# Kernel optimization log

Measured on AMD Instinct MI355X. Metric: run time of the kernel, lower is better.

The kernel has to match this reference:

```python
import jax, jax.numpy as jnp
import numpy as np

B, N, D = 4, 2048, 768
OUT = 768

def setup_inputs() -> dict:
    key = jax.random.key(0)
    k1, k2 = jax.random.split(key)
    x = jax.random.normal(k1, (B, N, D), dtype=jnp.float32)
    kernel = jax.random.normal(k2, (3, D, OUT), dtype=jnp.float32) * 0.02
    return {"x": x, "kernel": kernel}

def reference(x, kernel):
    # Single-head attention with shared QKV kernel stack [3, D, OUT]
    q = jnp.einsum('bnd,do->bno', x, kernel[0])
    k = jnp.einsum('bnd,do->bno', x, kernel[1])
    v = jnp.einsum('bnd,do->bno', x, kernel[2])
    # NOTE: original divides by 64**0.5 == 8 regardless of dims (faithful)
    scores = jnp.einsum('bqo,bko->bqk', q, k) / 8.0
    attn = jax.nn.softmax(scores, axis=-1)
    return jnp.einsum('bqk,bko->bqo', attn, v)
```

## Files before the change

### kernel.cpp

```cpp
#include <hip/hip_runtime.h>
#include <hip/hip_bf16.h>

constexpr int B_ = 4, N_ = 2048, D_ = 768, OUT_ = 768;
constexpr int M_ = B_ * N_;

typedef __attribute__((ext_vector_type(8))) short short8;
typedef __attribute__((ext_vector_type(4))) float floatx4;

__device__ __forceinline__ unsigned short f2bfu(float f) {
    union { __hip_bfloat16 b; unsigned short u; } cv;
    cv.b = __float2bfloat16(f);
    return cv.u;
}

#define GLOAD_LDS16(g, l)                                                     \
    __builtin_amdgcn_global_load_lds(                                         \
        (const __attribute__((address_space(1))) void*)(g),                   \
        (__attribute__((address_space(3))) void*)(l), 16, 0, 0)

#define MFMA_BF16 __builtin_amdgcn_mfma_f32_16x16x32_bf16
#define WAIT_LGKM0 asm volatile("s_waitcnt lgkmcnt(0)" ::: "memory")


template <int NT>
__device__ __forceinline__ void gemm4p(
    const __hip_bfloat16* __restrict__ aG, int lda,
    const __hip_bfloat16* __restrict__ bG, int ldb,
    unsigned short* LDS, floatx4 (&acc)[8][4]) {
    constexpr int ASLOT = 8192, BSLOT = 8192, BUFS = 32768;
    const int tid = threadIdx.x;
    const int wave = tid >> 6, lane = tid & 63;
    const int lrow = lane & 15, kq = lane >> 4;
    const int wm = (wave >> 2) * 128, wn = (wave & 3) * 64;

    const __hip_bfloat16 *sa0, *sa1, *sb0, *sb1;
    {
        const int r0 = tid >> 2, g0 = (tid & 3) ^ (r0 & 3);
        sa0 = aG + (size_t)r0 * lda + g0 * 8;
        sb0 = bG + (size_t)r0 * ldb + g0 * 8;
        const int u1 = 512 + tid, r1 = u1 >> 2, g1 = (u1 & 3) ^ (r1 & 3);
        sa1 = aG + (size_t)r1 * lda + g1 * 8;
        sb1 = bG + (size_t)r1 * ldb + g1 * 8;
    }
    int oa[8], ob[4];
#pragma unroll
    for (int i = 0; i < 8; ++i) {
        const int r = wm + i * 16 + lrow;
        oa[i] = r * 32 + ((kq ^ (r & 3)) * 8);
    }
#pragma unroll
    for (int i = 0; i < 4; ++i) {
        const int r = wn + i * 16 + lrow;
        ob[i] = r * 32 + ((kq ^ (r & 3)) * 8);
    }

#define SA4(tt, kh)                                                          \
    do {                                                                     \
        unsigned short* d_ =                                                 \
            LDS + ((tt) & 1) * BUFS + (kh) * ASLOT + wave * 512;             \
        GLOAD_LDS16(sa0 + (tt) * 64 + (kh) * 32, d_);                        \
        GLOAD_LDS16(sa1 + (tt) * 64 + (kh) * 32, d_ + 4096);                 \
    } while (0)
#define SB4(tt, kh)                                                          \
    do {                                                                     \
        unsigned short* d_ = LDS + ((tt) & 1) * BUFS + 2 * ASLOT +           \
                             (kh) * BSLOT + wave * 512;                      \
        GLOAD_LDS16(sb0 + (tt) * 64 + (kh) * 32, d_);                        \
        GLOAD_LDS16(sb1 + (tt) * 64 + (kh) * 32, d_ + 4096);                 \
    } while (0)

    SA4(0, 0); SB4(0, 0); SA4(0, 1); SB4(0, 1);
    SA4(1, 0); SB4(1, 0); SA4(1, 1);
    asm volatile("s_waitcnt vmcnt(6)" ::: "memory");
    __builtin_amdgcn_s_barrier();
    __builtin_amdgcn_sched_barrier(0);

    for (int t = 0; t < NT; ++t) {
        const unsigned short* Ab = LDS + (t & 1) * BUFS;
        const unsigned short* Bb = Ab + 2 * ASLOT;
        short8 af[8], bf0, bf1;
#pragma unroll
        for (int i = 0; i < 8; ++i) af[i] = *(const short8*)(Ab + oa[i]);
        bf0 = *(const short8*)(Bb + ob[0]);
        bf1 = *(const short8*)(Bb + ob[1]);
        if (t + 1 < NT) SB4(t + 1, 1);
        __builtin_amdgcn_s_barrier();
        WAIT_LGKM0;
        __builtin_amdgcn_sched_barrier(0);
        __builtin_amdgcn_s_setprio(1);
#pragma unroll
        for (int mi = 0; mi < 8; ++mi) {
            acc[mi][0] = MFMA_BF16(af[mi], bf0, acc[mi][0], 0, 0, 0);
            acc[mi][1] = MFMA_BF16(af[mi], bf1, acc[mi][1], 0, 0, 0);
        }
        __builtin_amdgcn_s_setprio(0);
        __builtin_amdgcn_s_barrier();
        bf0 = *(const short8*)(Bb + ob[2]);
        bf1 = *(const short8*)(Bb + ob[3]);
        if (t + 2 < NT) SA4(t + 2, 0);
        __builtin_amdgcn_s_barrier();
        WAIT_LGKM0;
        __builtin_amdgcn_sched_barrier(0);
        __builtin_amdgcn_s_setprio(1);
#pragma unroll
        for (int mi = 0; mi < 8; ++mi) {
            acc[mi][2] = MFMA_BF16(af[mi], bf0, acc[mi][2], 0, 0, 0);
            acc[mi][3] = MFMA_BF16(af[mi], bf1, acc[mi][3], 0, 0, 0);
        }
        __builtin_amdgcn_s_setprio(0);
        __builtin_amdgcn_s_barrier();
#pragma unroll
        for (int i = 0; i < 8; ++i)
            af[i] = *(const short8*)(Ab + ASLOT + oa[i]);
        bf0 = *(const short8*)(Bb + BSLOT + ob[2]);
        bf1 = *(const short8*)(Bb + BSLOT + ob[3]);
        if (t + 2 < NT) SB4(t + 2, 0);
        __builtin_amdgcn_s_barrier();
        WAIT_LGKM0;
        __builtin_amdgcn_sched_barrier(0);
        __builtin_amdgcn_s_setprio(1);
#pragma unroll
        for (int mi = 0; mi < 8; ++mi) {
            acc[mi][2] = MFMA_BF16(af[mi], bf0, acc[mi][2], 0, 0, 0);
            acc[mi][3] = MFMA_BF16(af[mi], bf1, acc[mi][3], 0, 0, 0);
        }
        __builtin_amdgcn_s_setprio(0);
        __builtin_amdgcn_s_barrier();
        bf0 = *(const short8*)(Bb + BSLOT + ob[0]);
        bf1 = *(const short8*)(Bb + BSLOT + ob[1]);
        if (t + 2 < NT) SA4(t + 2, 1);
        __builtin_amdgcn_s_barrier();
        WAIT_LGKM0;
        __builtin_amdgcn_sched_barrier(0);
        __builtin_amdgcn_s_setprio(1);
#pragma unroll
        for (int mi = 0; mi < 8; ++mi) {
            acc[mi][0] = MFMA_BF16(af[mi], bf0, acc[mi][0], 0, 0, 0);
            acc[mi][1] = MFMA_BF16(af[mi], bf1, acc[mi][1], 0, 0, 0);
        }
        __builtin_amdgcn_s_setprio(0);
        if (t + 2 < NT)
            asm volatile("s_waitcnt vmcnt(6)" ::: "memory");
        else if (t + 1 < NT)
            asm volatile("s_waitcnt vmcnt(0)" ::: "memory");
        __builtin_amdgcn_s_barrier();
        __builtin_amdgcn_sched_barrier(0);
    }
#undef SA4
#undef SB4
}

template <int NT>
__device__ __forceinline__ void gemm2p(
    const __hip_bfloat16* __restrict__ aG, int lda,
    const __hip_bfloat16* __restrict__ bG, int ldb,
    unsigned short* LDS, floatx4 (&acc)[4][4]) {
    constexpr int ASLOT = 4096, BSLOT = 8192, BUFS = 24576;
    const int tid = threadIdx.x;
    const int wave = tid >> 6, lane = tid & 63;
    const int lrow = lane & 15, kq = lane >> 4;
    const int wm = (wave >> 2) * 64, wn = (wave & 3) * 64;

    const __hip_bfloat16 *sa0, *sb0, *sb1;
    {
        const int r0 = tid >> 2, g0 = (tid & 3) ^ (r0 & 3);
        sa0 = aG + (size_t)r0 * lda + g0 * 8;
        sb0 = bG + (size_t)r0 * ldb + g0 * 8;
        const int u1 = 512 + tid, r1 = u1 >> 2, g1 = (u1 & 3) ^ (r1 & 3);
        sb1 = bG + (size_t)r1 * ldb + g1 * 8;
    }
    int oa[4], ob[4];
#pragma unroll
    for (int i = 0; i < 4; ++i) {
        const int ra = wm + i * 16 + lrow;
        oa[i] = ra * 32 + ((kq ^ (ra & 3)) * 8);
        const int rb = wn + i * 16 + lrow;
        ob[i] = rb * 32 + ((kq ^ (rb & 3)) * 8);
    }

#define SA2(tt, kh)                                                          \
    GLOAD_LDS16(sa0 + (tt) * 64 + (kh) * 32,                                 \
                LDS + ((tt) & 1) * BUFS + (kh) * ASLOT + wave * 512)
#define SB2(tt, kh)                                                          \
    do {                                                                     \
        unsigned short* d_ = LDS + ((tt) & 1) * BUFS + 2 * ASLOT +           \
                             (kh) * BSLOT + wave * 512;                      \
        GLOAD_LDS16(sb0 + (tt) * 64 + (kh) * 32, d_);                        \
        GLOAD_LDS16(sb1 + (tt) * 64 + (kh) * 32, d_ + 4096);                 \
    } while (0)

    SA2(0, 0); SB2(0, 0);
    SA2(0, 1); SB2(0, 1);
    SA2(1, 0); SB2(1, 0);
    asm volatile("s_waitcnt vmcnt(3)" ::: "memory");
    __builtin_amdgcn_s_barrier();
    __builtin_amdgcn_sched_barrier(0);

    for (int t = 0; t < NT; ++t) {
        const unsigned short* Ab = LDS + (t & 1) * BUFS;
        const unsigned short* Bb = Ab + 2 * ASLOT;
        short8 af[4], bf[4];
#pragma unroll
        for (int i = 0; i < 4; ++i) af[i] = *(const short8*)(Ab + oa[i]);
#pragma unroll
        for (int i = 0; i < 4; ++i) bf[i] = *(const short8*)(Bb + ob[i]);
        if (t + 1 < NT) { SA2(t + 1, 1); SB2(t + 1, 1); }
        __builtin_amdgcn_s_barrier();
        WAIT_LGKM0;
        __builtin_amdgcn_sched_barrier(0);
        __builtin_amdgcn_s_setprio(1);
#pragma unroll
        for (int mi = 0; mi < 4; ++mi)
#pragma unroll
            for (int ni = 0; ni < 4; ++ni)
                acc[mi][ni] = MFMA_BF16(af[mi], bf[ni], acc[mi][ni], 0, 0, 0);
        __builtin_amdgcn_s_setprio(0);
        __builtin_amdgcn_s_barrier();
#pragma unroll
        for (int i = 0; i < 4; ++i)
            af[i] = *(const short8*)(Ab + ASLOT + oa[i]);
#pragma unroll
        for (int i = 0; i < 4; ++i)
            bf[i] = *(const short8*)(Bb + BSLOT + ob[i]);
        if (t + 2 < NT) { SA2(t + 2, 0); SB2(t + 2, 0); }
        __builtin_amdgcn_s_barrier();
        WAIT_LGKM0;
        __builtin_amdgcn_sched_barrier(0);
        __builtin_amdgcn_s_setprio(1);
#pragma unroll
        for (int mi = 0; mi < 4; ++mi)
#pragma unroll
            for (int ni = 0; ni < 4; ++ni)
                acc[mi][ni] = MFMA_BF16(af[mi], bf[ni], acc[mi][ni], 0, 0, 0);
        __builtin_amdgcn_s_setprio(0);
        if (t + 2 < NT)
            asm volatile("s_waitcnt vmcnt(3)" ::: "memory");
        else if (t + 1 < NT)
            asm volatile("s_waitcnt vmcnt(0)" ::: "memory");
        __builtin_amdgcn_s_barrier();
        __builtin_amdgcn_sched_barrier(0);
    }
#undef SA2
#undef SB2
}

__global__ __launch_bounds__(256)
void prep(const float* __restrict__ x, const float* __restrict__ w,
          __hip_bfloat16* __restrict__ xb, __hip_bfloat16* __restrict__ wt,
          float* __restrict__ l) {
    __shared__ float t[32][33];
    const int tid = threadIdx.x;
    if (blockIdx.x < 3072) {
        const size_t i = (size_t)blockIdx.x * 2048 + (size_t)tid * 8;
        float4 a = *(const float4*)(x + i);
        float4 b = *(const float4*)(x + i + 4);
        *(ushort4*)((unsigned short*)xb + i) =
            make_ushort4(f2bfu(a.x), f2bfu(a.y), f2bfu(a.z), f2bfu(a.w));
        *(ushort4*)((unsigned short*)xb + i + 4) =
            make_ushort4(f2bfu(b.x), f2bfu(b.y), f2bfu(b.z), f2bfu(b.w));
    } else if (blockIdx.x < 4800) {
        const int bid = blockIdx.x - 3072;
        const int s = bid / 576, rem = bid % 576;
        const int d0 = (rem / 24) * 32, o0 = (rem % 24) * 32;
        const int tx = tid & 31, ty = tid >> 5;
        const float* ws = w + (size_t)s * D_ * OUT_;
        __hip_bfloat16* wts = wt + (size_t)s * OUT_ * D_;
#pragma unroll
        for (int i = 0; i < 4; ++i)
            t[ty + 8 * i][tx] = ws[(size_t)(d0 + ty + 8 * i) * OUT_ + o0 + tx];
        __syncthreads();
#pragma unroll
        for (int i = 0; i < 4; ++i)
            wts[(size_t)(o0 + ty + 8 * i) * D_ + d0 + tx] =
                __float2bfloat16(t[tx][ty + 8 * i]);
    } else {
        float4* l4 = (float4*)l;
#pragma unroll
        for (int i = 0; i < 8; ++i) l4[i * 256 + tid] = make_float4(0, 0, 0, 0);
    }
}

__global__ __launch_bounds__(512, 2)
void qkv_mfma(const __hip_bfloat16* __restrict__ xb,
              const __hip_bfloat16* __restrict__ wt,
              __hip_bfloat16* __restrict__ q, __hip_bfloat16* __restrict__ k,
              __hip_bfloat16* __restrict__ vt) {
    __shared__ __align__(16) unsigned short LDS[49152];
    const int s = blockIdx.z;
    const int m0 = blockIdx.x * 128, n0 = blockIdx.y * 256;
    floatx4 acc[4][4] = {};
    gemm2p<12>(xb + (size_t)m0 * D_, D_,
               wt + (size_t)s * OUT_ * D_ + (size_t)n0 * D_, D_, LDS, acc);

    const int tid = threadIdx.x, wave = tid >> 6, lane = tid & 63;
    const int lrow = lane & 15, kq = lane >> 4;
    const int wm = (wave >> 2) * 64, wn = (wave & 3) * 64;
    unsigned short* E = LDS;

    if (s < 2) {
        __syncthreads();
#pragma unroll
        for (int mi = 0; mi < 4; ++mi)
#pragma unroll
            for (int ni = 0; ni < 4; ++ni) {
                const int n = wn + ni * 16 + lrow;
#pragma unroll
                for (int r = 0; r < 4; ++r)
                    E[(wm + mi * 16 + kq * 4 + r) * 264 + n] =
                        f2bfu(acc[mi][ni][r]);
            }
        __syncthreads();
        unsigned short* outp = (unsigned short*)(s == 0 ? q : k);
#pragma unroll
        for (int i = 0; i < 8; ++i) {
            const int u = i * 512 + tid, row = u >> 5, c = u & 31;
            *(short8*)(outp + (size_t)(m0 + row) * OUT_ + n0 + c * 8) =
                *(const short8*)(E + row * 264 + c * 8);
        }
    } else {
        __syncthreads();
#pragma unroll
        for (int mi = 0; mi < 4; ++mi)
#pragma unroll
            for (int ni = 0; ni < 4; ++ni) {
                const int n = wn + ni * 16 + lrow;
#pragma unroll
                for (int r = 0; r < 4; ++r)
                    E[n * 136 + wm + mi * 16 + kq * 4 + r] =
                        f2bfu(acc[mi][ni][r]);
            }
        __syncthreads();
        const int b = m0 >> 11, j0 = m0 & 2047;
#pragma unroll
        for (int i = 0; i < 8; ++i) {
            const int u = i * 512 + tid, nr = u >> 4, c = u & 15;
            *(short8*)((unsigned short*)vt + ((size_t)b * OUT_ + n0 + nr) * N_ +
                       j0 + c * 8) = *(const short8*)(E + nr * 136 + c * 8);
        }
    }
}

__global__ __launch_bounds__(512, 2)
void scores_mfma(const __hip_bfloat16* __restrict__ q,
                 const __hip_bfloat16* __restrict__ k,
                 __hip_bfloat16* __restrict__ pt, float* __restrict__ l) {
    __shared__ __align__(16) unsigned short LDS[65536];
    const int b = blockIdx.z;
    const int m0 = blockIdx.x * 256, n0 = blockIdx.y * 256;
    floatx4 acc[8][4] = {};
    gemm4p<12>(q + (size_t)b * N_ * OUT_ + (size_t)m0 * OUT_, OUT_,
               k + (size_t)b * N_ * OUT_ + (size_t)n0 * OUT_, OUT_, LDS, acc);

    const int tid = threadIdx.x, wave = tid >> 6, lane = tid & 63;
    const int lrow = lane & 15, kq = lane >> 4;
    const int wm = (wave >> 2) * 128, wn = (wave & 3) * 64;

    float rs[8][4];
#pragma unroll
    for (int mi = 0; mi < 8; ++mi)
#pragma unroll
        for (int r = 0; r < 4; ++r) rs[mi][r] = 0.0f;
#pragma unroll
    for (int mi = 0; mi < 8; ++mi)
#pragma unroll
        for (int ni = 0; ni < 4; ++ni)
#pragma unroll
            for (int r = 0; r < 4; ++r) {
                const float e = __expf(acc[mi][ni][r] * 0.125f - 8.0f);
                acc[mi][ni][r] = e;
                rs[mi][r] += e;
            }
#pragma unroll
    for (int mi = 0; mi < 8; ++mi)
#pragma unroll
        for (int r = 0; r < 4; ++r) {
            float v = rs[mi][r];
            v += __shfl_xor(v, 1, 64);
            v += __shfl_xor(v, 2, 64);
            v += __shfl_xor(v, 4, 64);
            v += __shfl_xor(v, 8, 64);
            if (lrow == 0)
                atomicAdd(&l[(size_t)b * N_ + m0 + wm + mi * 16 + kq * 4 + r],
                          v);
        }

    unsigned short* E = LDS;
    unsigned short* pb = (unsigned short*)pt + (size_t)b * N_ * N_;
#pragma unroll
    for (int h = 0; h < 2; ++h) {
        __syncthreads();
        if ((wave >> 2) == h) {
#pragma unroll
            for (int mi = 0; mi < 8; ++mi)
#pragma unroll
                for (int ni = 0; ni < 4; ++ni) {
                    const int n = wn + ni * 16 + lrow;
#pragma unroll
                    for (int r = 0; r < 4; ++r)
                        E[(mi * 16 + kq * 4 + r) * 258 + n] =
                            f2bfu(acc[mi][ni][r]);
                }
        }
        __syncthreads();
#pragma unroll
        for (int i = 0; i < 8; ++i) {
            const int u = i * 512 + tid, row = u >> 5, c = u & 31;
            *(short8*)(pb + (size_t)(m0 + h * 128 + row) * N_ + n0 + c * 8) =
                *(const short8*)(E + row * 258 + c * 8);
        }
    }
}

__global__ __launch_bounds__(512, 2)
void pv_mfma(const __hip_bfloat16* __restrict__ pt,
             const __hip_bfloat16* __restrict__ vt,
             const float* __restrict__ l, float* __restrict__ out) {
    __shared__ __align__(16) unsigned short LDS[49152];
    const int b = blockIdx.z;
    const int m0 = blockIdx.x * 128, n0 = blockIdx.y * 256;
    floatx4 acc[4][4] = {};
    gemm2p<32>(pt + (size_t)b * N_ * N_ + (size_t)m0 * N_, N_,
               vt + (size_t)b * OUT_ * N_ + (size_t)n0 * N_, N_, LDS, acc);

    const int tid = threadIdx.x, wave = tid >> 6, lane = tid & 63;
    const int lrow = lane & 15, kq = lane >> 4;
    const int wm = (wave >> 2) * 64, wn = (wave & 3) * 64;
    const float* lb = l + (size_t)b * N_ + m0 + wm;
#pragma unroll
    for (int mi = 0; mi < 4; ++mi)
#pragma unroll
        for (int r = 0; r < 4; ++r) {
            const float inv = 1.0f / lb[mi * 16 + kq * 4 + r];
            float* o = out +
                       ((size_t)b * N_ + m0 + wm + mi * 16 + kq * 4 + r) *
                           OUT_ +
                       n0 + wn;
#pragma unroll
            for (int ni = 0; ni < 4; ++ni)
                o[ni * 16 + lrow] = acc[mi][ni][r] * inv;
        }
}

extern "C" void kernel_launch(void* const* d_in, const int* in_sizes, int n_in,
                              void* d_out, int out_size, void* d_ws,
                              size_t ws_size, hipStream_t stream) {
    const float* x = (const float*)d_in[0];
    const float* w = (const float*)d_in[1];
    float* out = (float*)d_out;

    __hip_bfloat16* q  = (__hip_bfloat16*)d_ws;
    __hip_bfloat16* k  = q + (size_t)M_ * OUT_;
    __hip_bfloat16* vt = k + (size_t)M_ * OUT_;
    __hip_bfloat16* xb = vt + (size_t)M_ * OUT_;
    __hip_bfloat16* wt = xb + (size_t)M_ * D_;
    float* l = (float*)(wt + (size_t)3 * OUT_ * D_);
    __hip_bfloat16* pt = (__hip_bfloat16*)(l + M_);

    prep<<<dim3(4801), dim3(256), 0, stream>>>(x, w, xb, wt, l);
    qkv_mfma<<<dim3(64, 3, 3), dim3(512), 0, stream>>>(xb, wt, q, k, vt);
    scores_mfma<<<dim3(8, 8, 4), dim3(512), 0, stream>>>(q, k, pt, l);
    pv_mfma<<<dim3(16, 3, 4), dim3(512), 0, stream>>>(pt, vt, l, out);
}
```

Measured before the change: 201.5 us.

## Restructure GEMM LDS staging to 64-wide k tiles with triple buffering

Rewrites the shared GEMM mainloops so each k-step's A and B tiles land in one 64-column LDS slab with an 8-way XOR swizzle, replacing the old split into two 32-column halves. The 2-panel GEMM used by the QKV and PV kernels becomes a three-buffer ring that prefetches two steps ahead, with one load group per step instead of split half-loads. The 4-panel GEMM reorders its fragment reads and prefetch points to match the new layout. The goal is fewer barriers and waits per k-step and deeper load/compute overlap. The cost is larger LDS (144KB per block for QKV/PV), which may reduce occupancy below the requested two blocks per CU.

After: 194.1 us. -3.7%, faster.

```diff
diff --git a/kernel.cpp b/kernel.cpp
--- a/kernel.cpp
+++ b/kernel.cpp
@@ -20,6 +20,9 @@
 
 #define MFMA_BF16 __builtin_amdgcn_mfma_f32_16x16x32_bf16
 #define WAIT_LGKM0 asm volatile("s_waitcnt lgkmcnt(0)" ::: "memory")
+#define SBAR __builtin_amdgcn_s_barrier
+#define SCHED0 __builtin_amdgcn_sched_barrier
+#define PRIO __builtin_amdgcn_s_setprio
 
 
 template <int NT>
@@ -27,221 +30,211 @@
     const __hip_bfloat16* __restrict__ aG, int lda,
     const __hip_bfloat16* __restrict__ bG, int ldb,
     unsigned short* LDS, floatx4 (&acc)[8][4]) {
-    constexpr int ASLOT = 8192, BSLOT = 8192, BUFS = 32768;
     const int tid = threadIdx.x;
     const int wave = tid >> 6, lane = tid & 63;
     const int lrow = lane & 15, kq = lane >> 4;
     const int wm = (wave >> 2) * 128, wn = (wave & 3) * 64;
 
-    const __hip_bfloat16 *sa0, *sa1, *sb0, *sb1;
-    {
-        const int r0 = tid >> 2, g0 = (tid & 3) ^ (r0 & 3);
-        sa0 = aG + (size_t)r0 * lda + g0 * 8;
-        sb0 = bG + (size_t)r0 * ldb + g0 * 8;
-        const int u1 = 512 + tid, r1 = u1 >> 2, g1 = (u1 & 3) ^ (r1 & 3);
-        sa1 = aG + (size_t)r1 * lda + g1 * 8;
-        sb1 = bG + (size_t)r1 * ldb + g1 * 8;
-    }
-    int oa[8], ob[4];
-#pragma unroll
-    for (int i = 0; i < 8; ++i) {
-        const int r = wm + i * 16 + lrow;
-        oa[i] = r * 32 + ((kq ^ (r & 3)) * 8);
-    }
-#pragma unroll
-    for (int i = 0; i < 4; ++i) {
-        const int r = wn + i * 16 + lrow;
-        ob[i] = r * 32 + ((kq ^ (r & 3)) * 8);
-    }
-
-#define SA4(tt, kh)                                                          \
+    const int rr = tid >> 3;
+    const int colg = ((tid & 7) ^ (rr & 7)) * 8;
+    const __hip_bfloat16* pa[4];
+    const __hip_bfloat16* pb[4];
+#pragma unroll
+    for (int j = 0; j < 4; ++j) {
+        pa[j] = aG + (size_t)(j * 64 + rr) * lda + colg;
+        pb[j] = bG + (size_t)(j * 64 + rr) * ldb + colg;
+    }
+    const int s0 = (kq ^ (lrow & 7)) * 8, s1 = ((4 + kq) ^ (lrow & 7)) * 8;
+    const int arow = (wm + lrow) * 64, brow = (wn + lrow) * 64;
+
+#define SA_(tt)                                                              \
     do {                                                                     \
-        unsigned short* d_ =                                                 \
-            LDS + ((tt) & 1) * BUFS + (kh) * ASLOT + wave * 512;             \
-        GLOAD_LDS16(sa0 + (tt) * 64 + (kh) * 32, d_);                        \
-        GLOAD_LDS16(sa1 + (tt) * 64 + (kh) * 32, d_ + 4096);                 \
+        unsigned short* d_ = LDS + ((tt) & 1) * 32768 + wave * 512;          \
+        GLOAD_LDS16(pa[0] + (tt) * 64, d_);                                  \
+        GLOAD_LDS16(pa[1] + (tt) * 64, d_ + 4096);                           \
+        GLOAD_LDS16(pa[2] + (tt) * 64, d_ + 8192);                           \
+        GLOAD_LDS16(pa[3] + (tt) * 64, d_ + 12288);                          \
     } while (0)
-#define SB4(tt, kh)                                                          \
+#define SB_(tt)                                                              \
     do {                                                                     \
-        unsigned short* d_ = LDS + ((tt) & 1) * BUFS + 2 * ASLOT +           \
-                             (kh) * BSLOT + wave * 512;                      \
-        GLOAD_LDS16(sb0 + (tt) * 64 + (kh) * 32, d_);                        \
-        GLOAD_LDS16(sb1 + (tt) * 64 + (kh) * 32, d_ + 4096);                 \
+        unsigned short* d_ = LDS + ((tt) & 1) * 32768 + 16384 + wave * 512;  \
+        GLOAD_LDS16(pb[0] + (tt) * 64, d_);                                  \
+        GLOAD_LDS16(pb[1] + (tt) * 64, d_ + 4096);                           \
+        GLOAD_LDS16(pb[2] + (tt) * 64, d_ + 8192);                           \
+        GLOAD_LDS16(pb[3] + (tt) * 64, d_ + 12288);                          \
     } while (0)
 
-    SA4(0, 0); SB4(0, 0); SA4(0, 1); SB4(0, 1);
-    SA4(1, 0); SB4(1, 0); SA4(1, 1);
+    SA_(0); SB_(0); SB_(1);
+    asm volatile("s_waitcnt vmcnt(4)" ::: "memory");
+    SBAR();
+    SCHED0(0);
+
+    for (int t = 0; t < NT; ++t) {
+        unsigned short* Ab = LDS + (t & 1) * 32768;
+        unsigned short* Bb = Ab + 16384;
+        const unsigned short* pA0 = Ab + arow + s0;
+        const unsigned short* pA1 = Ab + arow + s1;
+        const unsigned short* pB0 = Bb + brow + s0;
+        const unsigned short* pB1 = Bb + brow + s1;
+        short8 af[8], b00, b01, b02, b03, b10, b11, b12, b13;
+#pragma unroll
+        for (int mi = 0; mi < 8; ++mi)
+            af[mi] = *(const short8*)(pA0 + mi * 1024);
+        b00 = *(const short8*)(pB0);
+        b01 = *(const short8*)(pB0 + 1024);
+        if (t + 1 < NT) SA_(t + 1);
+        SBAR();
+        WAIT_LGKM0;
+        SCHED0(0);
+        PRIO(1);
+#pragma unroll
+        for (int mi = 0; mi < 8; ++mi) {
+            acc[mi][0] = MFMA_BF16(af[mi], b00, acc[mi][0], 0, 0, 0);
+            acc[mi][1] = MFMA_BF16(af[mi], b01, acc[mi][1], 0, 0, 0);
+        }
+        PRIO(0);
+        SBAR();
+        b02 = *(const short8*)(pB0 + 2048);
+        b03 = *(const short8*)(pB0 + 3072);
+        b10 = *(const short8*)(pB1);
+        b11 = *(const short8*)(pB1 + 1024);
+        SBAR();
+        WAIT_LGKM0;
+        SCHED0(0);
+        PRIO(1);
+#pragma unroll
+        for (int mi = 0; mi < 8; ++mi) {
+            acc[mi][2] = MFMA_BF16(af[mi], b02, acc[mi][2], 0, 0, 0);
+            acc[mi][3] = MFMA_BF16(af[mi], b03, acc[mi][3], 0, 0, 0);
+        }
+        PRIO(0);
+        SBAR();
+#pragma unroll
+        for (int mi = 0; mi < 8; ++mi)
+            af[mi] = *(const short8*)(pA1 + mi * 1024);
+        b12 = *(const short8*)(pB1 + 2048);
+        b13 = *(const short8*)(pB1 + 3072);
+        SBAR();
+        WAIT_LGKM0;
+        SCHED0(0);
+        PRIO(1);
+#pragma unroll
+        for (int mi = 0; mi < 8; ++mi) {
+            acc[mi][0] = MFMA_BF16(af[mi], b10, acc[mi][0], 0, 0, 0);
+            acc[mi][1] = MFMA_BF16(af[mi], b11, acc[mi][1], 0, 0, 0);
+        }
+        PRIO(0);
+        SBAR();
+        if (t + 2 < NT) SB_(t + 2);
+        SCHED0(0);
+        PRIO(1);
+#pragma unroll
+        for (int mi = 0; mi < 8; ++mi) {
+            acc[mi][2] = MFMA_BF16(af[mi], b12, acc[mi][2], 0, 0, 0);
+            acc[mi][3] = MFMA_BF16(af[mi], b13, acc[mi][3], 0, 0, 0);
+        }
+        PRIO(0);
+        if (t + 2 < NT)
+            asm volatile("s_waitcnt vmcnt(4)" ::: "memory");
+        else if (t + 1 < NT)
+            asm volatile("s_waitcnt vmcnt(0)" ::: "memory");
+        SBAR();
+        SCHED0(0);
+    }
+#undef SA_
+#undef SB_
+}
+
+template <int NT>
+__device__ __forceinline__ void gemm2p3(
+    const __hip_bfloat16* __restrict__ aG, int lda,
+    const __hip_bfloat16* __restrict__ bG, int ldb,
+    unsigned short* LDS, floatx4 (&acc)[4][4]) {
+    const int tid = threadIdx.x;
+    const int wave = tid >> 6, lane = tid & 63;
+    const int lrow = lane & 15, kq = lane >> 4;
+    const int wm = (wave >> 2) * 64, wn = (wave & 3) * 64;
+
+    const int rr = tid >> 3;
+    const int colg = ((tid & 7) ^ (rr & 7)) * 8;
+    const __hip_bfloat16* pa[2];
+    const __hip_bfloat16* pb[4];
+#pragma unroll
+    for (int j = 0; j < 2; ++j)
+        pa[j] = aG + (size_t)(j * 64 + rr) * lda + colg;
+#pragma unroll
+    for (int j = 0; j < 4; ++j)
+        pb[j] = bG + (size_t)(j * 64 + rr) * ldb + colg;
+
+    const int s0 = (kq ^ (lrow & 7)) * 8, s1 = ((4 + kq) ^ (lrow & 7)) * 8;
+    const int arow = (wm + lrow) * 64, brow = (wn + lrow) * 64;
+
+#define ST_(tt, base)                                                        \
+    do {                                                                     \
+        unsigned short* d_ = LDS + (base) + wave * 512;                      \
+        GLOAD_LDS16(pa[0] + (tt) * 64, d_);                                  \
+        GLOAD_LDS16(pa[1] + (tt) * 64, d_ + 4096);                           \
+        GLOAD_LDS16(pb[0] + (tt) * 64, d_ + 8192);                           \
+        GLOAD_LDS16(pb[1] + (tt) * 64, d_ + 12288);                          \
+        GLOAD_LDS16(pb[2] + (tt) * 64, d_ + 16384);                          \
+        GLOAD_LDS16(pb[3] + (tt) * 64, d_ + 20480);                          \
+    } while (0)
+
+    ST_(0, 0);
+    ST_(1, 24576);
     asm volatile("s_waitcnt vmcnt(6)" ::: "memory");
-    __builtin_amdgcn_s_barrier();
-    __builtin_amdgcn_sched_barrier(0);
-
+    SBAR();
+    SCHED0(0);
+
+    int rb = 0, sb = 2;
     for (int t = 0; t < NT; ++t) {
-        const unsigned short* Ab = LDS + (t & 1) * BUFS;
-        const unsigned short* Bb = Ab + 2 * ASLOT;
-        short8 af[8], bf0, bf1;
-#pragma unroll
-        for (int i = 0; i < 8; ++i) af[i] = *(const short8*)(Ab + oa[i]);
-        bf0 = *(const short8*)(Bb + ob[0]);
-        bf1 = *(const short8*)(Bb + ob[1]);
-        if (t + 1 < NT) SB4(t + 1, 1);
-        __builtin_amdgcn_s_barrier();
+        unsigned short* Ab = LDS + rb * 24576;
+        unsigned short* Bb = Ab + 8192;
+        const unsigned short* pA0 = Ab + arow + s0;
+        const unsigned short* pA1 = Ab + arow + s1;
+        const unsigned short* pB0 = Bb + brow + s0;
+        const unsigned short* pB1 = Bb + brow + s1;
+        short8 a[4], b[4];
+#pragma unroll
+        for (int i = 0; i < 4; ++i) a[i] = *(const short8*)(pA0 + i * 1024);
+#pragma unroll
+        for (int i = 0; i < 4; ++i) b[i] = *(const short8*)(pB0 + i * 1024);
+        if (t + 2 < NT) ST_(t + 2, sb * 24576);
+        SBAR();
         WAIT_LGKM0;
-        __builtin_amdgcn_sched_barrier(0);
-        __builtin_amdgcn_s_setprio(1);
-#pragma unroll
-        for (int mi = 0; mi < 8; ++mi) {
-            acc[mi][0] = MFMA_BF16(af[mi], bf0, acc[mi][0], 0, 0, 0);
-            acc[mi][1] = MFMA_BF16(af[mi], bf1, acc[mi][1], 0, 0, 0);
-        }
-        __builtin_amdgcn_s_setprio(0);
-        __builtin_amdgcn_s_barrier();
-        bf0 = *(const short8*)(Bb + ob[2]);
-        bf1 = *(const short8*)(Bb + ob[3]);
-        if (t + 2 < NT) SA4(t + 2, 0);
-        __builtin_amdgcn_s_barrier();
+        SCHED0(0);
+        PRIO(1);
+#pragma unroll
+        for (int mi = 0; mi < 4; ++mi)
+#pragma unroll
+            for (int ni = 0; ni < 4; ++ni)
+                acc[mi][ni] = MFMA_BF16(a[mi], b[ni], acc[mi][ni], 0, 0, 0);
+        PRIO(0);
+        SBAR();
+#pragma unroll
+        for (int i = 0; i < 4; ++i) a[i] = *(const short8*)(pA1 + i * 1024);
+#pragma unroll
+        for (int i = 0; i < 4; ++i) b[i] = *(const short8*)(pB1 + i * 1024);
+        SBAR();
         WAIT_LGKM0;
-        __builtin_amdgcn_sched_barrier(0);
-        __builtin_amdgcn_s_setprio(1);
-#pragma unroll
-        for (int mi = 0; mi < 8; ++mi) {
-            acc[mi][2] = MFMA_BF16(af[mi], bf0, acc[mi][2], 0, 0, 0);
-            acc[mi][3] = MFMA_BF16(af[mi], bf1, acc[mi][3], 0, 0, 0);
-        }
-        __builtin_amdgcn_s_setprio(0);
-        __builtin_amdgcn_s_barrier();
-#pragma unroll
-        for (int i = 0; i < 8; ++i)
-            af[i] = *(const short8*)(Ab + ASLOT + oa[i]);
-        bf0 = *(const short8*)(Bb + BSLOT + ob[2]);
-        bf1 = *(const short8*)(Bb + BSLOT + ob[3]);
-        if (t + 2 < NT) SB4(t + 2, 0);
-        __builtin_amdgcn_s_barrier();
-        WAIT_LGKM0;
-        __builtin_amdgcn_sched_barrier(0);
-        __builtin_amdgcn_s_setprio(1);
-#pragma unroll
-        for (int mi = 0; mi < 8; ++mi) {
-            acc[mi][2] = MFMA_BF16(af[mi], bf0, acc[mi][2], 0, 0, 0);
-            acc[mi][3] = MFMA_BF16(af[mi], bf1, acc[mi][3], 0, 0, 0);
-        }
-        __builtin_amdgcn_s_setprio(0);
-        __builtin_amdgcn_s_barrier();
-        bf0 = *(const short8*)(Bb + BSLOT + ob[0]);
-        bf1 = *(const short8*)(Bb + BSLOT + ob[1]);
-        if (t + 2 < NT) SA4(t + 2, 1);
-        __builtin_amdgcn_s_barrier();
-        WAIT_LGKM0;
-        __builtin_amdgcn_sched_barrier(0);
-        __builtin_amdgcn_s_setprio(1);
-#pragma unroll
-        for (int mi = 0; mi < 8; ++mi) {
-            acc[mi][0] = MFMA_BF16(af[mi], bf0, acc[mi][0], 0, 0, 0);
-            acc[mi][1] = MFMA_BF16(af[mi], bf1, acc[mi][1], 0, 0, 0);
-        }
-        __builtin_amdgcn_s_setprio(0);
+        SCHED0(0);
+        PRIO(1);
+#pragma unroll
+        for (int mi = 0; mi < 4; ++mi)
+#pragma unroll
+            for (int ni = 0; ni < 4; ++ni)
+                acc[mi][ni] = MFMA_BF16(a[mi], b[ni], acc[mi][ni], 0, 0, 0);
+        PRIO(0);
         if (t + 2 < NT)
             asm volatile("s_waitcnt vmcnt(6)" ::: "memory");
         else if (t + 1 < NT)
             asm volatile("s_waitcnt vmcnt(0)" ::: "memory");
-        __builtin_amdgcn_s_barrier();
-        __builtin_amdgcn_sched_barrier(0);
-    }
-#undef SA4
-#undef SB4
-}
-
-template <int NT>
-__device__ __forceinline__ void gemm2p(
-    const __hip_bfloat16* __restrict__ aG, int lda,
-    const __hip_bfloat16* __restrict__ bG, int ldb,
-    unsigned short* LDS, floatx4 (&acc)[4][4]) {
-    constexpr int ASLOT = 4096, BSLOT = 8192, BUFS = 24576;
-    const int tid = threadIdx.x;
-    const int wave = tid >> 6, lane = tid & 63;
-    const int lrow = lane & 15, kq = lane >> 4;
-    const int wm = (wave >> 2) * 64, wn = (wave & 3) * 64;
-
-    const __hip_bfloat16 *sa0, *sb0, *sb1;
-    {
-        const int r0 = tid >> 2, g0 = (tid & 3) ^ (r0 & 3);
-        sa0 = aG + (size_t)r0 * lda + g0 * 8;
-        sb0 = bG + (size_t)r0 * ldb + g0 * 8;
-        const int u1 = 512 + tid, r1 = u1 >> 2, g1 = (u1 & 3) ^ (r1 & 3);
-        sb1 = bG + (size_t)r1 * ldb + g1 * 8;
-    }
-    int oa[4], ob[4];
-#pragma unroll
-    for (int i = 0; i < 4; ++i) {
-        const int ra = wm + i * 16 + lrow;
-        oa[i] = ra * 32 + ((kq ^ (ra & 3)) * 8);
-        const int rb = wn + i * 16 + lrow;
-        ob[i] = rb * 32 + ((kq ^ (rb & 3)) * 8);
-    }
-
-#define SA2(tt, kh)                                                          \
-    GLOAD_LDS16(sa0 + (tt) * 64 + (kh) * 32,                                 \
-                LDS + ((tt) & 1) * BUFS + (kh) * ASLOT + wave * 512)
-#define SB2(tt, kh)                                                          \
-    do {                                                                     \
-        unsigned short* d_ = LDS + ((tt) & 1) * BUFS + 2 * ASLOT +           \
-                             (kh) * BSLOT + wave * 512;                      \
-        GLOAD_LDS16(sb0 + (tt) * 64 + (kh) * 32, d_);                        \
-        GLOAD_LDS16(sb1 + (tt) * 64 + (kh) * 32, d_ + 4096);                 \
-    } while (0)
-
-    SA2(0, 0); SB2(0, 0);
-    SA2(0, 1); SB2(0, 1);
-    SA2(1, 0); SB2(1, 0);
-    asm volatile("s_waitcnt vmcnt(3)" ::: "memory");
-    __builtin_amdgcn_s_barrier();
-    __builtin_amdgcn_sched_barrier(0);
-
-    for (int t = 0; t < NT; ++t) {
-        const unsigned short* Ab = LDS + (t & 1) * BUFS;
-        const unsigned short* Bb = Ab + 2 * ASLOT;
-        short8 af[4], bf[4];
-#pragma unroll
-        for (int i = 0; i < 4; ++i) af[i] = *(const short8*)(Ab + oa[i]);
-#pragma unroll
-        for (int i = 0; i < 4; ++i) bf[i] = *(const short8*)(Bb + ob[i]);
-        if (t + 1 < NT) { SA2(t + 1, 1); SB2(t + 1, 1); }
-        __builtin_amdgcn_s_barrier();
-        WAIT_LGKM0;
-        __builtin_amdgcn_sched_barrier(0);
-        __builtin_amdgcn_s_setprio(1);
-#pragma unroll
-        for (int mi = 0; mi < 4; ++mi)
-#pragma unroll
-            for (int ni = 0; ni < 4; ++ni)
-                acc[mi][ni] = MFMA_BF16(af[mi], bf[ni], acc[mi][ni], 0, 0, 0);
-        __builtin_amdgcn_s_setprio(0);
-        __builtin_amdgcn_s_barrier();
-#pragma unroll
-        for (int i = 0; i < 4; ++i)
-            af[i] = *(const short8*)(Ab + ASLOT + oa[i]);
-#pragma unroll
-        for (int i = 0; i < 4; ++i)
-            bf[i] = *(const short8*)(Bb + BSLOT + ob[i]);
-        if (t + 2 < NT) { SA2(t + 2, 0); SB2(t + 2, 0); }
-        __builtin_amdgcn_s_barrier();
-        WAIT_LGKM0;
-        __builtin_amdgcn_sched_barrier(0);
-        __builtin_amdgcn_s_setprio(1);
-#pragma unroll
-        for (int mi = 0; mi < 4; ++mi)
-#pragma unroll
-            for (int ni = 0; ni < 4; ++ni)
-                acc[mi][ni] = MFMA_BF16(af[mi], bf[ni], acc[mi][ni], 0, 0, 0);
-        __builtin_amdgcn_s_setprio(0);
-        if (t + 2 < NT)
-            asm volatile("s_waitcnt vmcnt(3)" ::: "memory");
-        else if (t + 1 < NT)
-            asm volatile("s_waitcnt vmcnt(0)" ::: "memory");
-        __builtin_amdgcn_s_barrier();
-        __builtin_amdgcn_sched_barrier(0);
-    }
-#undef SA2
-#undef SB2
+        SBAR();
+        SCHED0(0);
+        rb = (rb == 2) ? 0 : rb + 1;
+        sb = (sb == 2) ? 0 : sb + 1;
+    }
+#undef ST_
 }
 
 __global__ __launch_bounds__(256)
@@ -285,12 +278,12 @@
               const __hip_bfloat16* __restrict__ wt,
               __hip_bfloat16* __restrict__ q, __hip_bfloat16* __restrict__ k,
               __hip_bfloat16* __restrict__ vt) {
-    __shared__ __align__(16) unsigned short LDS[49152];
+    __shared__ __align__(16) unsigned short LDS[73728];
     const int s = blockIdx.z;
     const int m0 = blockIdx.x * 128, n0 = blockIdx.y * 256;
     floatx4 acc[4][4] = {};
-    gemm2p<12>(xb + (size_t)m0 * D_, D_,
-               wt + (size_t)s * OUT_ * D_ + (size_t)n0 * D_, D_, LDS, acc);
+    gemm2p3<12>(xb + (size_t)m0 * D_, D_,
+                wt + (size_t)s * OUT_ * D_ + (size_t)n0 * D_, D_, LDS, acc);
 
     const int tid = threadIdx.x, wave = tid >> 6, lane = tid & 63;
     const int lrow = lane & 15, kq = lane >> 4;
@@ -415,12 +408,12 @@
 void pv_mfma(const __hip_bfloat16* __restrict__ pt,
              const __hip_bfloat16* __restrict__ vt,
              const float* __restrict__ l, float* __restrict__ out) {
-    __shared__ __align__(16) unsigned short LDS[49152];
+    __shared__ __align__(16) unsigned short LDS[73728];
     const int b = blockIdx.z;
     const int m0 = blockIdx.x * 128, n0 = blockIdx.y * 256;
     floatx4 acc[4][4] = {};
-    gemm2p<32>(pt + (size_t)b * N_ * N_ + (size_t)m0 * N_, N_,
-               vt + (size_t)b * OUT_ * N_ + (size_t)n0 * N_, N_, LDS, acc);
+    gemm2p3<32>(pt + (size_t)b * N_ * N_ + (size_t)m0 * N_, N_,
+                vt + (size_t)b * OUT_ * N_ + (size_t)n0 * N_, N_, LDS, acc);
 
     const int tid = threadIdx.x, wave = tid >> 6, lane = tid & 63;
     const int lrow = lane & 15, kq = lane >> 4;
```
